# Kernel optimization log

Measured on AMD Instinct MI355X. Metric: run time of the kernel, lower is better.

## Reference

```python
import jax, jax.numpy as jnp
import numpy as np

N_NODES = 40000
N_EDGES = 640000
F_IN = 128
F_OUT = 128
K_HOPS = 2


def setup_inputs() -> dict:
    key = jax.random.key(0)
    k1, k2, k3, k4 = jax.random.split(key, 4)
    x = jax.random.normal(k1, (N_NODES, F_IN), dtype=jnp.float32)
    edge_index = jax.random.randint(k2, (2, N_EDGES), 0, N_NODES, dtype=jnp.int64)
    edge_weight = jax.random.uniform(k3, (N_EDGES,), dtype=jnp.float32)
    # Linear(in_feats, out_feats): weight [F_OUT, F_IN], bias [F_OUT]
    W = jax.random.normal(k4, (F_OUT, F_IN), dtype=jnp.float32) * (1.0 / np.sqrt(F_IN))
    b = jnp.zeros((F_OUT,), dtype=jnp.float32)
    return {"x": x, "edge_index": edge_index, "edge_weight": edge_weight, "W": W, "b": b}


def reference(x, edge_index, edge_weight, W, b):
    N = x.shape[0]
    # gcn_norm with add_self_loops=True, fill_value=1.0
    loop = jnp.arange(N, dtype=edge_index.dtype)
    row = jnp.concatenate([edge_index[0], loop])  # source (j)
    col = jnp.concatenate([edge_index[1], loop])  # target (i)
    w = jnp.concatenate([edge_weight, jnp.ones((N,), dtype=edge_weight.dtype)])
    deg = jax.ops.segment_sum(w, col, num_segments=N)
    deg_inv_sqrt = jnp.where(deg > 0, jax.lax.rsqrt(jnp.maximum(deg, 1e-30)), 0.0)
    norm = deg_inv_sqrt[row] * w * deg_inv_sqrt[col]  # [E+N]
    # K-hop propagation: x <- A_norm @ x, repeated K times
    for _ in range(K_HOPS):
        msgs = norm[:, None] * x[row]  # [E+N, F]
        x = jax.ops.segment_sum(msgs, col, num_segments=N)
    # final linear
    return x @ W.T + b
```

## Files before the change

### kernel.cpp

```cpp
#include <hip/hip_runtime.h>
#include <hip/hip_fp16.h>


#define F    128
#define CAP  64
#define EPB  4096
#define BPT  16

typedef _Float16 f16x8 __attribute__((ext_vector_type(8)));
typedef float    f32x4 __attribute__((ext_vector_type(4)));

__global__ __launch_bounds__(256) void prep_kernel(
    const float2* __restrict__ x2in, __half2* __restrict__ xh, int npairs,
    const int* __restrict__ ei, const float* __restrict__ ew,
    uint2* __restrict__ coarse, int* __restrict__ cnt1, int E,
    int nbin, int nb1,
    const float2* __restrict__ W2, __half2* __restrict__ Wh2,
    int buildBlocks, int cvtBlocks) {
    int b = blockIdx.x;
    if (b < buildBlocks) {
        __shared__ int binCnt[256];
        int t = threadIdx.x;
        if (t < nbin) binCnt[t] = 0;
        __syncthreads();
        int base = b * EPB;
        unsigned rc[BPT]; unsigned short hw[BPT];
        #pragma unroll
        for (int j = 0; j < BPT; ++j) {
            int e = base + j * 256 + t;
            bool v = e < E;
            int   r = v ? ei[e]     : 0;
            int   c = v ? ei[E + e] : 0;
            float w = v ? ew[e]     : 0.f;
            rc[j] = v ? ((unsigned)r | ((unsigned)c << 16)) : 0xFFFFFFFFu;
            hw[j] = __half_as_ushort(__float2half(w));
        }
        #pragma unroll
        for (int j = 0; j < BPT; ++j) {
            if (rc[j] == 0xFFFFFFFFu) continue;
            int c   = (int)(rc[j] >> 16);
            int bin = c >> 8;
            int rank = atomicAdd(&binCnt[bin], 1);
            if (rank < CAP) {
                uint2 ent;
                ent.x = (rc[j] & 0xFFFFu) | ((unsigned)hw[j] << 16);
                ent.y = (unsigned)(c & 0xFF);
                coarse[((size_t)bin * nb1 + b) * CAP + rank] = ent;
            }
        }
        __syncthreads();
        if (t < nbin) cnt1[(size_t)b * nbin + t] = min(binCnt[t], CAP);
    } else if (b < buildBlocks + cvtBlocks) {
        int idx = (b - buildBlocks) * 256 + threadIdx.x;
        if (idx < npairs) xh[idx] = __float22half2_rn(x2in[idx]);
    } else {
        int idx = (b - buildBlocks - cvtBlocks) * 256 + threadIdx.x;
        if (idx < F * F / 2) Wh2[idx] = __float22half2_rn(W2[idx]);
    }
}

__global__ __launch_bounds__(1024) void finalize_kernel(
    const uint2* __restrict__ coarse, const int* __restrict__ cnt1,
    unsigned int* __restrict__ bucket, int* __restrict__ cnt,
    float* __restrict__ dinv, int N, int nbin, int nb1) {
    __shared__ int   nodeCnt[256];
    __shared__ float degS[256];
    __shared__ int   c1s[256];
    int b = blockIdx.x;
    int t = threadIdx.x;
    if (t < 256) {
        nodeCnt[t] = 0;
        degS[t]    = 0.f;
    }
    for (int i = t; i < nb1; i += 1024) c1s[i] = cnt1[(size_t)i * nbin + b];
    __syncthreads();
    int tot = nb1 * CAP;
    for (int s = t; s < tot; s += 1024) {
        int blk = s >> 6, slot = s & 63;
        if (slot < c1s[blk]) {
            uint2 ent = coarse[((size_t)b * nb1 + blk) * CAP + slot];
            int local = (int)(ent.y & 0xFFu);
            int rank  = atomicAdd(&nodeCnt[local], 1);
            float wf  = __half2float(__ushort_as_half((unsigned short)(ent.x >> 16)));
            atomicAdd(&degS[local], wf);
            if (rank < CAP)
                bucket[(((size_t)b << 8) | (unsigned)local) * CAP + rank] = ent.x;
        }
    }
    __syncthreads();
    int node = (b << 8) + t;
    if (t < 256 && node < N) {
        cnt[node]  = min(nodeCnt[t], CAP);
        dinv[node] = 1.0f / sqrtf(degS[t] + 1.0f);
    }
}

__global__ __launch_bounds__(256) void hop_kernel(
    const unsigned short* __restrict__ xin, unsigned short* __restrict__ xout,
    const float* __restrict__ dinv, const unsigned int* __restrict__ bucket,
    const int* __restrict__ cnt) {
    int t = threadIdx.x;
    int lane = t & 63;
    int wid  = t >> 6;
    int q = lane & 31;
    int h = lane >> 5;
    int i = blockIdx.x * 8 + wid * 2 + h;

    int c = min(cnt[i], CAP);
    float di = dinv[i];
    int r0 = i, r1 = i;
    float n0 = 0.0f, n1 = 0.0f;
    if (q < c) {
        unsigned int ent = bucket[i * CAP + q];
        r0 = (int)(ent & 0xFFFFu);
        float w = __half2float(__ushort_as_half((unsigned short)(ent >> 16)));
        n0 = di * dinv[r0] * w;
    }
    if (q + 32 < c) {
        unsigned int ent = bucket[i * CAP + q + 32];
        r1 = (int)(ent & 0xFFFFu);
        float w = __half2float(__ushort_as_half((unsigned short)(ent >> 16)));
        n1 = di * dinv[r1] * w;
    }
    int cmax = max(c, __shfl_xor(c, 32, 64));

    uint2 sv = *(const uint2*)(xin + (size_t)i * F + q * 4);
    float2 slo = __half22float2(*(const __half2*)&sv.x);
    float2 shi = __half22float2(*(const __half2*)&sv.y);
    float dii = di * di;
    float4 acc = make_float4(dii * slo.x, dii * slo.y, dii * shi.x, dii * shi.y);

    int kend1 = cmax < 32 ? cmax : 32;
    int k = 0;
    for (; k + 8 <= kend1; k += 8) {
        int rr[8]; float nn[8]; uint2 v[8];
        #pragma unroll
        for (int j = 0; j < 8; ++j) {
            rr[j] = __shfl(r0, k + j, 32);
            nn[j] = __shfl(n0, k + j, 32);
        }
        #pragma unroll
        for (int j = 0; j < 8; ++j)
            v[j] = *(const uint2*)(xin + (size_t)rr[j] * F + q * 4);
        #pragma unroll
        for (int j = 0; j < 8; ++j) {
            float2 lo = __half22float2(*(const __half2*)&v[j].x);
            float2 hi = __half22float2(*(const __half2*)&v[j].y);
            acc.x += nn[j] * lo.x; acc.y += nn[j] * lo.y;
            acc.z += nn[j] * hi.x; acc.w += nn[j] * hi.y;
        }
    }
    for (; k < kend1; ++k) {
        int   rk = __shfl(r0, k, 32);
        float nk = __shfl(n0, k, 32);
        uint2 v  = *(const uint2*)(xin + (size_t)rk * F + q * 4);
        float2 lo = __half22float2(*(const __half2*)&v.x);
        float2 hi = __half22float2(*(const __half2*)&v.y);
        acc.x += nk * lo.x; acc.y += nk * lo.y;
        acc.z += nk * hi.x; acc.w += nk * hi.y;
    }
    for (; k + 8 <= cmax; k += 8) {
        int rr[8]; float nn[8]; uint2 v[8];
        #pragma unroll
        for (int j = 0; j < 8; ++j) {
            rr[j] = __shfl(r1, k - 32 + j, 32);
            nn[j] = __shfl(n1, k - 32 + j, 32);
        }
        #pragma unroll
        for (int j = 0; j < 8; ++j)
            v[j] = *(const uint2*)(xin + (size_t)rr[j] * F + q * 4);
        #pragma unroll
        for (int j = 0; j < 8; ++j) {
            float2 lo = __half22float2(*(const __half2*)&v[j].x);
            float2 hi = __half22float2(*(const __half2*)&v[j].y);
            acc.x += nn[j] * lo.x; acc.y += nn[j] * lo.y;
            acc.z += nn[j] * hi.x; acc.w += nn[j] * hi.y;
        }
    }
    for (; k < cmax; ++k) {
        int   rk = __shfl(r1, k - 32, 32);
        float nk = __shfl(n1, k - 32, 32);
        uint2 v  = *(const uint2*)(xin + (size_t)rk * F + q * 4);
        float2 lo = __half22float2(*(const __half2*)&v.x);
        float2 hi = __half22float2(*(const __half2*)&v.y);
        acc.x += nk * lo.x; acc.y += nk * lo.y;
        acc.z += nk * hi.x; acc.w += nk * hi.y;
    }

    uint2 o;
    *(__half2*)&o.x = __float22half2_rn(make_float2(acc.x, acc.y));
    *(__half2*)&o.y = __float22half2_rn(make_float2(acc.z, acc.w));
    *(uint2*)&xout[(size_t)i * F + q * 4] = o;
}

__global__ __launch_bounds__(256) void linear_mfma_kernel(
    const unsigned short* __restrict__ x2h, const unsigned short* __restrict__ Wh,
    const float* __restrict__ bias, float* __restrict__ out) {
    int t = threadIdx.x;
    int lane = t & 63;
    int wid  = t >> 6;
    int m    = lane & 15;
    int quad = lane >> 4;
    int n0 = blockIdx.x * 64 + wid * 16;

    f32x4 acc[8];
    #pragma unroll
    for (int ft = 0; ft < 8; ++ft) acc[ft] = (f32x4){0.f, 0.f, 0.f, 0.f};

    #pragma unroll
    for (int ks = 0; ks < 4; ++ks) {
        f16x8 a = *(const f16x8*)(x2h + (size_t)(n0 + m) * F + ks * 32 + quad * 8);
        #pragma unroll
        for (int ft = 0; ft < 8; ++ft) {
            f16x8 b = *(const f16x8*)(Wh + (size_t)(ft * 16 + m) * F + ks * 32 + quad * 8);
            acc[ft] = __builtin_amdgcn_mfma_f32_16x16x32_f16(a, b, acc[ft], 0, 0, 0);
        }
    }
    #pragma unroll
    for (int ft = 0; ft < 8; ++ft) {
        int f = ft * 16 + m;
        float bv = bias[f];
        #pragma unroll
        for (int reg = 0; reg < 4; ++reg) {
            int n = n0 + quad * 4 + reg;
            out[(size_t)n * F + f] = acc[ft][reg] + bv;
        }
    }
}

extern "C" void kernel_launch(void* const* d_in, const int* in_sizes, int n_in,
                              void* d_out, int out_size, void* d_ws, size_t ws_size,
                              hipStream_t stream) {
    const float* x    = (const float*)d_in[0];
    const int*   ei   = (const int*)d_in[1];
    const float* ew   = (const float*)d_in[2];
    const float* W    = (const float*)d_in[3];
    const float* bias = (const float*)d_in[4];
    float* out = (float*)d_out;

    const int N = in_sizes[0] / F;
    const int E = in_sizes[2];

    const int nbin = (N + 255) >> 8;
    const int nb1  = (E + EPB - 1) / EPB;

    char* ws = (char*)d_ws;
    size_t off = 0;
    auto take = [&](size_t bytes) {
        size_t r = off;
        off = (off + bytes + 255) & ~(size_t)255;
        return r;
    };
    size_t o_cnt1   = take((size_t)nb1 * nbin * 4);
    size_t o_coarse = take((size_t)nbin * nb1 * CAP * 8);
    size_t o_cnt    = take((size_t)N * 4);
    size_t o_dinv   = take((size_t)N * 4);
    size_t o_bucket = take((size_t)N * CAP * 4);
    size_t o_xh     = take((size_t)N * F * 2);
    size_t o_x1h    = take((size_t)N * F * 2);
    size_t o_x2h    = take((size_t)N * F * 2);
    size_t o_wh     = take((size_t)F * F * 2);
    (void)ws_size;

    int*            cnt1   = (int*)(ws + o_cnt1);
    uint2*          coarse = (uint2*)(ws + o_coarse);
    int*            cnt    = (int*)(ws + o_cnt);
    float*          dinv   = (float*)(ws + o_dinv);
    unsigned int*   bucket = (unsigned int*)(ws + o_bucket);
    __half2*        xh2    = (__half2*)(ws + o_xh);
    unsigned short* xh     = (unsigned short*)(ws + o_xh);
    unsigned short* x1h    = (unsigned short*)(ws + o_x1h);
    unsigned short* x2h    = (unsigned short*)(ws + o_x2h);
    __half2*        wh2    = (__half2*)(ws + o_wh);
    unsigned short* wh     = (unsigned short*)(ws + o_wh);

    int npairs = N * 64;
    int cvtBlocks = (npairs + 255) / 256;
    int wBlocks   = (F * F / 2 + 255) / 256;
    prep_kernel<<<nb1 + cvtBlocks + wBlocks, 256, 0, stream>>>(
        (const float2*)x, xh2, npairs, ei, ew, coarse, cnt1, E, nbin, nb1,
        (const float2*)W, wh2, nb1, cvtBlocks);
    finalize_kernel<<<nbin, 1024, 0, stream>>>(coarse, cnt1, bucket, cnt, dinv,
                                               N, nbin, nb1);
    hop_kernel<<<N / 8, 256, 0, stream>>>(xh,  x1h, dinv, bucket, cnt);
    hop_kernel<<<N / 8, 256, 0, stream>>>(x1h, x2h, dinv, bucket, cnt);
    linear_mfma_kernel<<<N / 64, 256, 0, stream>>>(x2h, wh, bias, out);
}
```

Baseline: 163.2 us.

## Fuse second propagation hop with final linear layer via LDS tile and MFMA

The second hop now aggregates 16 nodes per 512-thread block and writes the fp16 results into a padded shared-memory tile. Eight waves then each compute one 16-column slice of the output with MFMA and add the bias, so the intermediate x2h buffer is never written to or read back from global memory, and one kernel launch goes away. The cost is a larger block with a __syncthreads, which can reduce how well the gather latency is hidden. W is also read per block at a much finer granularity.

```diff
diff --git a/kernel.cpp b/kernel.cpp
--- a/kernel.cpp
+++ b/kernel.cpp
@@ -6,6 +6,7 @@
 #define CAP  64
 #define EPB  4096
 #define BPT  16
+#define TPAD 136
 
 typedef _Float16 f16x8 __attribute__((ext_vector_type(8)));
 typedef float    f32x4 __attribute__((ext_vector_type(4)));
@@ -193,38 +194,123 @@
     *(uint2*)&xout[(size_t)i * F + q * 4] = o;
 }
 
-__global__ __launch_bounds__(256) void linear_mfma_kernel(
-    const unsigned short* __restrict__ x2h, const unsigned short* __restrict__ Wh,
-    const float* __restrict__ bias, float* __restrict__ out) {
+__global__ __launch_bounds__(512) void hop_linear_kernel(
+    const unsigned short* __restrict__ xin, const unsigned short* __restrict__ Wh,
+    const float* __restrict__ bias, float* __restrict__ out,
+    const float* __restrict__ dinv, const unsigned int* __restrict__ bucket,
+    const int* __restrict__ cnt) {
+    __shared__ unsigned short tile[16][TPAD];
     int t = threadIdx.x;
     int lane = t & 63;
     int wid  = t >> 6;
+    int q = lane & 31;
+    int h = lane >> 5;
+    int row = wid * 2 + h;
+    int i = blockIdx.x * 16 + row;
+
+    int c = min(cnt[i], CAP);
+    float di = dinv[i];
+    int r0 = i, r1 = i;
+    float n0 = 0.0f, n1 = 0.0f;
+    if (q < c) {
+        unsigned int ent = bucket[i * CAP + q];
+        r0 = (int)(ent & 0xFFFFu);
+        float w = __half2float(__ushort_as_half((unsigned short)(ent >> 16)));
+        n0 = di * dinv[r0] * w;
+    }
+    if (q + 32 < c) {
+        unsigned int ent = bucket[i * CAP + q + 32];
+        r1 = (int)(ent & 0xFFFFu);
+        float w = __half2float(__ushort_as_half((unsigned short)(ent >> 16)));
+        n1 = di * dinv[r1] * w;
+    }
+    int cmax = max(c, __shfl_xor(c, 32, 64));
+
+    uint2 sv = *(const uint2*)(xin + (size_t)i * F + q * 4);
+    float2 slo = __half22float2(*(const __half2*)&sv.x);
+    float2 shi = __half22float2(*(const __half2*)&sv.y);
+    float dii = di * di;
+    float4 acc = make_float4(dii * slo.x, dii * slo.y, dii * shi.x, dii * shi.y);
+
+    int kend1 = cmax < 32 ? cmax : 32;
+    int k = 0;
+    for (; k + 8 <= kend1; k += 8) {
+        int rr[8]; float nn[8]; uint2 v[8];
+        #pragma unroll
+        for (int j = 0; j < 8; ++j) {
+            rr[j] = __shfl(r0, k + j, 32);
+            nn[j] = __shfl(n0, k + j, 32);
+        }
+        #pragma unroll
+        for (int j = 0; j < 8; ++j)
+            v[j] = *(const uint2*)(xin + (size_t)rr[j] * F + q * 4);
+        #pragma unroll
+        for (int j = 0; j < 8; ++j) {
+            float2 lo = __half22float2(*(const __half2*)&v[j].x);
+            float2 hi = __half22float2(*(const __half2*)&v[j].y);
+            acc.x += nn[j] * lo.x; acc.y += nn[j] * lo.y;
+            acc.z += nn[j] * hi.x; acc.w += nn[j] * hi.y;
+        }
+    }
+    for (; k < kend1; ++k) {
+        int   rk = __shfl(r0, k, 32);
+        float nk = __shfl(n0, k, 32);
+        uint2 v  = *(const uint2*)(xin + (size_t)rk * F + q * 4);
+        float2 lo = __half22float2(*(const __half2*)&v.x);
+        float2 hi = __half22float2(*(const __half2*)&v.y);
+        acc.x += nk * lo.x; acc.y += nk * lo.y;
+        acc.z += nk * hi.x; acc.w += nk * hi.y;
+    }
+    for (; k + 8 <= cmax; k += 8) {
+        int rr[8]; float nn[8]; uint2 v[8];
+        #pragma unroll
+        for (int j = 0; j < 8; ++j) {
+            rr[j] = __shfl(r1, k - 32 + j, 32);
+            nn[j] = __shfl(n1, k - 32 + j, 32);
+        }
+        #pragma unroll
+        for (int j = 0; j < 8; ++j)
+            v[j] = *(const uint2*)(xin + (size_t)rr[j] * F + q * 4);
+        #pragma unroll
+        for (int j = 0; j < 8; ++j) {
+            float2 lo = __half22float2(*(const __half2*)&v[j].x);
+            float2 hi = __half22float2(*(const __half2*)&v[j].y);
+            acc.x += nn[j] * lo.x; acc.y += nn[j] * lo.y;
+            acc.z += nn[j] * hi.x; acc.w += nn[j] * hi.y;
+        }
+    }
+    for (; k < cmax; ++k) {
+        int   rk = __shfl(r1, k - 32, 32);
+        float nk = __shfl(n1, k - 32, 32);
+        uint2 v  = *(const uint2*)(xin + (size_t)rk * F + q * 4);
+        float2 lo = __half22float2(*(const __half2*)&v.x);
+        float2 hi = __half22float2(*(const __half2*)&v.y);
+        acc.x += nk * lo.x; acc.y += nk * lo.y;
+        acc.z += nk * hi.x; acc.w += nk * hi.y;
+    }
+
+    uint2 o;
+    *(__half2*)&o.x = __float22half2_rn(make_float2(acc.x, acc.y));
+    *(__half2*)&o.y = __float22half2_rn(make_float2(acc.z, acc.w));
+    *(uint2*)&tile[row][q * 4] = o;
+    __syncthreads();
+
     int m    = lane & 15;
     int quad = lane >> 4;
-    int n0 = blockIdx.x * 64 + wid * 16;
-
-    f32x4 acc[8];
-    #pragma unroll
-    for (int ft = 0; ft < 8; ++ft) acc[ft] = (f32x4){0.f, 0.f, 0.f, 0.f};
-
+    f32x4 acc2 = (f32x4){0.f, 0.f, 0.f, 0.f};
     #pragma unroll
     for (int ks = 0; ks < 4; ++ks) {
-        f16x8 a = *(const f16x8*)(x2h + (size_t)(n0 + m) * F + ks * 32 + quad * 8);
-        #pragma unroll
-        for (int ft = 0; ft < 8; ++ft) {
-            f16x8 b = *(const f16x8*)(Wh + (size_t)(ft * 16 + m) * F + ks * 32 + quad * 8);
-            acc[ft] = __builtin_amdgcn_mfma_f32_16x16x32_f16(a, b, acc[ft], 0, 0, 0);
-        }
-    }
+        f16x8 a = *(const f16x8*)&tile[m][ks * 32 + quad * 8];
+        f16x8 b = *(const f16x8*)(Wh + (size_t)(wid * 16 + m) * F + ks * 32 + quad * 8);
+        acc2 = __builtin_amdgcn_mfma_f32_16x16x32_f16(a, b, acc2, 0, 0, 0);
+    }
+    int n0b = blockIdx.x * 16;
+    int f = wid * 16 + m;
+    float bv = bias[f];
     #pragma unroll
-    for (int ft = 0; ft < 8; ++ft) {
-        int f = ft * 16 + m;
-        float bv = bias[f];
-        #pragma unroll
-        for (int reg = 0; reg < 4; ++reg) {
-            int n = n0 + quad * 4 + reg;
-            out[(size_t)n * F + f] = acc[ft][reg] + bv;
-        }
+    for (int reg = 0; reg < 4; ++reg) {
+        int n = n0b + quad * 4 + reg;
+        out[(size_t)n * F + f] = acc2[reg] + bv;
     }
 }
 
@@ -258,7 +344,6 @@
     size_t o_bucket = take((size_t)N * CAP * 4);
     size_t o_xh     = take((size_t)N * F * 2);
     size_t o_x1h    = take((size_t)N * F * 2);
-    size_t o_x2h    = take((size_t)N * F * 2);
     size_t o_wh     = take((size_t)F * F * 2);
     (void)ws_size;
 
@@ -270,7 +355,6 @@
     __half2*        xh2    = (__half2*)(ws + o_xh);
     unsigned short* xh     = (unsigned short*)(ws + o_xh);
     unsigned short* x1h    = (unsigned short*)(ws + o_x1h);
-    unsigned short* x2h    = (unsigned short*)(ws + o_x2h);
     __half2*        wh2    = (__half2*)(ws + o_wh);
     unsigned short* wh     = (unsigned short*)(ws + o_wh);
 
@@ -282,7 +366,7 @@
         (const float2*)W, wh2, nb1, cvtBlocks);
     finalize_kernel<<<nbin, 1024, 0, stream>>>(coarse, cnt1, bucket, cnt, dinv,
                                                N, nbin, nb1);
-    hop_kernel<<<N / 8, 256, 0, stream>>>(xh,  x1h, dinv, bucket, cnt);
-    hop_kernel<<<N / 8, 256, 0, stream>>>(x1h, x2h, dinv, bucket, cnt);
-    linear_mfma_kernel<<<N / 64, 256, 0, stream>>>(x2h, wh, bias, out);
-}
+    hop_kernel<<<N / 8, 256, 0, stream>>>(xh, x1h, dinv, bucket, cnt);
+    hop_linear_kernel<<<N / 16, 512, 0, stream>>>(x1h, wh, bias, out,
+                                                  dinv, bucket, cnt);
+}
```

New measurement: 158.7 us, median of 2. 1.03x faster.
